# Kernel optimization log

Measured on AMD Instinct MI355X. Metric: run time of the kernel, lower is better.

The kernel has to match this reference:

```python
import jax, jax.numpy as jnp
import numpy as np

N_AGENT = 25
N_S = 32
N_A = 4
HID = 128
EHH_HID = HID * N_AGENT          # 3200
INTER = 150                      # INTERMEDIATE_NODES
BATCH = 2048
N_EDGE = 300


def _leaky(x):
    return jnp.where(x >= 0, x, 0.01 * x)


def setup_inputs() -> dict:
    key = jax.random.key(0)
    ks = jax.random.split(key, 12)
    states = jax.random.normal(ks[0], (N_AGENT, BATCH, N_S), dtype=jnp.float32)
    ehh_w = jax.random.normal(ks[1], (N_AGENT * N_S, EHH_HID), dtype=jnp.float32) * 0.05
    anova = jax.random.normal(ks[2], (EHH_HID + INTER, N_AGENT), dtype=jnp.float32)
    w1 = jax.random.normal(ks[3], (N_AGENT, EHH_HID, 12), dtype=jnp.float32) * 0.02
    b1 = jax.random.normal(ks[4], (N_AGENT, 12), dtype=jnp.float32) * 0.02
    w2 = jax.random.normal(ks[5], (N_AGENT, 12, 12), dtype=jnp.float32) * 0.3
    b2 = jax.random.normal(ks[6], (N_AGENT, 12), dtype=jnp.float32) * 0.02
    w3 = jax.random.normal(ks[7], (N_AGENT, 12, N_A), dtype=jnp.float32) * 0.3
    b3 = jax.random.normal(ks[8], (N_AGENT, N_A), dtype=jnp.float32) * 0.02
    actions = jax.random.randint(ks[9], (N_AGENT, BATCH), 0, N_A, dtype=jnp.int32)
    # adjacency rows: (bi_att_row, neighbor_row_a, unused, neighbor_row_b)
    c0 = jax.random.randint(ks[10], (N_EDGE, 1), 0, INTER, dtype=jnp.int32)
    c13 = jax.random.randint(ks[11], (N_EDGE, 2), 0, EHH_HID, dtype=jnp.int32)
    adj = jnp.concatenate([c0, c13[:, :1], jnp.zeros((N_EDGE, 1), jnp.int32), c13[:, 1:]], axis=1)
    return {"states": states, "ehh_w": ehh_w, "anova": anova,
            "w1": w1, "b1": b1, "w2": w2, "b2": b2, "w3": w3, "b3": b3,
            "actions": actions, "adj": adj}


def reference(states, ehh_w, anova, w1, b1, w2, b2, w3, b3, actions, adj):
    # states: (A, B, S) -> ehh_s: (B, A*S)   (torch.cat(states, dim=1))
    B = states.shape[1]
    ehh_s = jnp.transpose(states, (1, 0, 2)).reshape(B, -1)
    # EHH normalization (BatchNorm, affine=False, batch stats) + linear + LeakyReLU
    mu = jnp.mean(ehh_s, axis=0, keepdims=True)
    var = jnp.var(ehh_s, axis=0, keepdims=True)
    ehh_n = (ehh_s - mu) * jax.lax.rsqrt(var + 1e-5)
    ehh_embedding = _leaky(ehh_n @ ehh_w)                    # (B, EHH_HID)

    # ANOVA attention assembly via adjacency scatter
    self_att = anova[:EHH_HID, :]                            # (EHH_HID, A)
    bi_att = anova[EHH_HID:, :]                              # (INTER, A)
    vals = bi_att[adj[:, 0], :]                              # (E, A)
    neighbor_att = jnp.zeros((EHH_HID, N_AGENT), jnp.float32)
    neighbor_att = neighbor_att.at[adj[:, 1]].set(vals)
    neighbor_att = neighbor_att.at[adj[:, 3]].set(vals)
    all_att = (self_att + neighbor_att).T                    # (A, EHH_HID)

    # att_s repeat/permute/reshape == broadcast of embedding per agent
    att_out = ehh_embedding[:, None, :] * all_att[None, :, :]  # (B, A, EHH_HID)

    # per-agent critics (ehh_hidden -> 12 -> 12 -> n_a)
    h1 = _leaky(jnp.einsum('bah,ahk->bak', att_out, w1) + b1[None])
    h2 = _leaky(jnp.einsum('bak,akj->baj', h1, w2) + b2[None])
    all_q = jnp.einsum('baj,ajc->bac', h2, w3) + b3[None]     # (B, A, N_A)

    # q = all_q.gather(1, in_acs) per agent -> (A, B)
    q = jnp.take_along_axis(all_q, actions.T[:, :, None], axis=2)[..., 0].T
    return q
```

## Files before the change

kernel.cpp:

```cpp
#include <hip/hip_runtime.h>
#include <cstdint>

#define NAG 25
#define NS 32
#define EHH 3200
#define KDIM 800
#define BATCH 2048
#define NEDGE 300
#define NPAD 384
#define KSPLIT 5

typedef _Float16 half8 __attribute__((ext_vector_type(8)));
typedef float f32x4 __attribute__((ext_vector_type(4)));

__device__ __forceinline__ float leaky(float x) { return x >= 0.f ? x : 0.01f * x; }

__global__ void init_kernel(float* __restrict__ acc, int* __restrict__ winner) {
    int t = blockIdx.x * 256 + threadIdx.x;
    if (t < 1600) acc[t] = 0.f;
    if (t < EHH) winner[t] = -1;
}

__global__ void stats_part(const float* __restrict__ states, float* __restrict__ acc) {
    int a = blockIdx.x;
    int chunk = blockIdx.y;
    int s = threadIdx.x & 31, ty = threadIdx.x >> 5;
    const float* base = states + ((size_t)a * BATCH + chunk * 128) * NS + s;
    float sum = 0.f, sq = 0.f;
    for (int b = ty; b < 128; b += 8) {
        float v = base[(size_t)b * NS];
        sum += v; sq += v * v;
    }
    __shared__ float ls[8][32], lq[8][32];
    ls[ty][s] = sum; lq[ty][s] = sq;
    __syncthreads();
    if (ty == 0) {
#pragma unroll
        for (int i = 1; i < 8; ++i) { sum += ls[i][s]; sq += lq[i][s]; }
        atomicAdd(&acc[a * 32 + s], sum);
        atomicAdd(&acc[800 + a * 32 + s], sq);
    }
}

__global__ void prep_kernel(const float* __restrict__ states, const float* __restrict__ acc,
                            const float* __restrict__ ehh_w, const int* __restrict__ adj,
                            int* __restrict__ winner,
                            _Float16* __restrict__ A, _Float16* __restrict__ wt) {
    __shared__ float tile[32][33];
    int bi = blockIdx.x;
    if (bi < 6400) {
        int t = bi * 256 + threadIdx.x;
        int b = t / KDIM;
        int f = t - b * KDIM;
        int a = f >> 5, s = f & 31;
        float m = acc[f] * (1.f / BATCH);
        float var = acc[800 + f] * (1.f / BATCH) - m * m;
        float rs = rsqrtf(var + 1e-5f);
        float v = states[((size_t)a * BATCH + b) * NS + s];
        A[t] = (_Float16)((v - m) * rs);
    } else if (bi < 8900) {
        int bb = bi - 6400;
        int n0 = (bb % 100) * 32, k0 = (bb / 100) * 32;
        int x = threadIdx.x & 31, y = threadIdx.x >> 5;
        for (int i = y; i < 32; i += 8)
            tile[i][x] = ehh_w[(size_t)(k0 + i) * EHH + n0 + x];
        __syncthreads();
        for (int i = y; i < 32; i += 8)
            wt[(size_t)(n0 + i) * KDIM + k0 + x] = (_Float16)tile[x][i];
    } else {
        int e = (bi - 8900) * 256 + threadIdx.x;
        if (e < 2 * NEDGE) {
            int pass = e >= NEDGE;
            int ee = pass ? e - NEDGE : e;
            int dest = adj[ee * 4 + (pass ? 3 : 1)];
            atomicMax(&winner[dest], e);
        }
    }
}

__global__ void w2d_kernel(const float* __restrict__ anova, const int* __restrict__ adj,
                           const int* __restrict__ winner, const float* __restrict__ w1,
                           _Float16* __restrict__ w2dt) {
    if (blockIdx.x < 313) {
        int t = blockIdx.x * 256 + threadIdx.x;
        if (t < NAG * EHH) {
            int a = t / EHH;
            int h = t - a * EHH;
            float att = anova[(size_t)h * NAG + a];
            int w = winner[h];
            if (w >= 0) {
                int ee = w >= NEDGE ? w - NEDGE : w;
                att += anova[(size_t)(EHH + adj[ee * 4]) * NAG + a];
            }
            const float* wp = w1 + ((size_t)a * EHH + h) * 12;
#pragma unroll
            for (int kk = 0; kk < 12; ++kk)
                w2dt[(size_t)(a * 12 + kk) * EHH + h] = (_Float16)(att * wp[kk]);
        }
    } else {
        int p = (blockIdx.x - 313) * 256 + threadIdx.x;
        if (p < (NPAD - 300) * EHH / 8) {
            half8 z = {0, 0, 0, 0, 0, 0, 0, 0};
            ((half8*)(w2dt + (size_t)300 * EHH))[p] = z;
        }
    }
}

__device__ __forceinline__ void async16(const void* g, void* l) {
    __builtin_amdgcn_global_load_lds(
        (const __attribute__((address_space(1))) void*)(uintptr_t)g,
        (__attribute__((address_space(3))) void*)(unsigned)(uintptr_t)l, 16, 0, 0);
}

template <bool LEAKY_F16_OUT>
__global__ __launch_bounds__(256)
void gemm_bt(const _Float16* __restrict__ A, const _Float16* __restrict__ B,
             _Float16* __restrict__ Ch, float* __restrict__ Cf,
             int Ktot, int ldc, int kPerSplit, int slabStride) {
    __shared__ __attribute__((aligned(16))) _Float16 As[2][128 * 32];
    __shared__ __attribute__((aligned(16))) _Float16 Bs[2][128 * 32];
    const int tid = threadIdx.x;
    const int lane = tid & 63;
    const int wave = tid >> 6;
    const int wm = (wave >> 1) << 6;
    const int wn = (wave & 1) << 6;
    const int m0 = blockIdx.x << 7;
    const int n0 = blockIdx.y << 7;
    const int k0 = blockIdx.z * kPerSplit;
    const int nk = kPerSplit >> 5;

    const int srow = lane >> 2;
    const int scol = (lane & 3) << 3;
    const _Float16* gA0 = A + (size_t)(m0 + wave * 16 + srow) * Ktot + k0 + scol;
    const _Float16* gA1 = gA0 + (size_t)64 * Ktot;
    const _Float16* gB0 = B + (size_t)(n0 + wave * 16 + srow) * Ktot + k0 + scol;
    const _Float16* gB1 = gB0 + (size_t)64 * Ktot;
    const int lofs = wave * 512;

    f32x4 acc[4][4];
    const f32x4 zero = {0.f, 0.f, 0.f, 0.f};
#pragma unroll
    for (int i = 0; i < 4; ++i)
#pragma unroll
        for (int j = 0; j < 4; ++j) acc[i][j] = zero;

    const int fr = lane & 15;
    const int q8 = (lane >> 4) << 3;

    async16(gA0, As[0] + lofs);
    async16(gA1, As[0] + 2048 + lofs);
    async16(gB0, Bs[0] + lofs);
    async16(gB1, Bs[0] + 2048 + lofs);

    for (int kt = 0; kt < nk; ++kt) {
        const int cur = kt & 1;
        __syncthreads();
        if (kt + 1 < nk) {
            const int ko = (kt + 1) << 5;
            const int nxt = cur ^ 1;
            async16(gA0 + ko, As[nxt] + lofs);
            async16(gA1 + ko, As[nxt] + 2048 + lofs);
            async16(gB0 + ko, Bs[nxt] + lofs);
            async16(gB1 + ko, Bs[nxt] + 2048 + lofs);
        }
        half8 av[4], bv[4];
#pragma unroll
        for (int i = 0; i < 4; ++i)
            av[i] = *(const half8*)(As[cur] + (wm + i * 16 + fr) * 32 + q8);
#pragma unroll
        for (int j = 0; j < 4; ++j)
            bv[j] = *(const half8*)(Bs[cur] + (wn + j * 16 + fr) * 32 + q8);
#pragma unroll
        for (int i = 0; i < 4; ++i)
#pragma unroll
            for (int j = 0; j < 4; ++j)
                acc[i][j] = __builtin_amdgcn_mfma_f32_16x16x32_f16(av[i], bv[j], acc[i][j], 0, 0, 0);
    }

    const int r0 = (lane >> 4) << 2;
    if (LEAKY_F16_OUT) {
#pragma unroll
        for (int i = 0; i < 4; ++i)
#pragma unroll
            for (int j = 0; j < 4; ++j)
#pragma unroll
                for (int r = 0; r < 4; ++r) {
                    int row = m0 + wm + i * 16 + r0 + r;
                    int col = n0 + wn + j * 16 + fr;
                    Ch[(size_t)row * ldc + col] = (_Float16)leaky(acc[i][j][r]);
                }
    } else {
        float* C = Cf + (size_t)blockIdx.z * slabStride;
#pragma unroll
        for (int i = 0; i < 4; ++i)
#pragma unroll
            for (int j = 0; j < 4; ++j)
#pragma unroll
                for (int r = 0; r < 4; ++r) {
                    int row = m0 + wm + i * 16 + r0 + r;
                    int col = n0 + wn + j * 16 + fr;
                    C[(size_t)row * ldc + col] = acc[i][j][r];
                }
    }
}

__global__ void tail_kernel(const float* __restrict__ Hp, const float* __restrict__ b1,
                            const float* __restrict__ w2, const float* __restrict__ b2,
                            const float* __restrict__ w3, const float* __restrict__ b3,
                            const int* __restrict__ act, float* __restrict__ out) {
    int t = blockIdx.x * 256 + threadIdx.x;
    int b = t & (BATCH - 1);
    int a = t >> 11;
    const float* hp = Hp + (size_t)b * NPAD + a * 12;
    float h1[12];
#pragma unroll
    for (int k = 0; k < 12; ++k) {
        float s = b1[a * 12 + k];
#pragma unroll
        for (int ks = 0; ks < KSPLIT; ++ks) s += hp[(size_t)ks * BATCH * NPAD + k];
        h1[k] = leaky(s);
    }
    float h2[12];
#pragma unroll
    for (int j = 0; j < 12; ++j) {
        float s = b2[a * 12 + j];
#pragma unroll
        for (int k = 0; k < 12; ++k) s += h1[k] * w2[(a * 12 + k) * 12 + j];
        h2[j] = leaky(s);
    }
    int c = act[t];
    float q = b3[a * 4 + c];
#pragma unroll
    for (int j = 0; j < 12; ++j) q += h2[j] * w3[(a * 12 + j) * 4 + c];
    out[t] = q;
}

extern "C" void kernel_launch(void* const* d_in, const int* in_sizes, int n_in,
                              void* d_out, int out_size, void* d_ws, size_t ws_size,
                              hipStream_t stream) {
    (void)in_sizes; (void)n_in; (void)out_size; (void)ws_size;
    const float* states = (const float*)d_in[0];
    const float* ehh_w  = (const float*)d_in[1];
    const float* anova  = (const float*)d_in[2];
    const float* w1     = (const float*)d_in[3];
    const float* b1     = (const float*)d_in[4];
    const float* w2     = (const float*)d_in[5];
    const float* b2     = (const float*)d_in[6];
    const float* w3     = (const float*)d_in[7];
    const float* b3     = (const float*)d_in[8];
    const int* actions  = (const int*)d_in[9];
    const int* adj      = (const int*)d_in[10];
    float* out = (float*)d_out;

    char* ws = (char*)d_ws;
    float*     acc    = (float*)    (ws + 0);
    int*       winner = (int*)      (ws + 8192);
    _Float16*  Abf    = (_Float16*) (ws + 32768);
    _Float16*  WbT    = (_Float16*) (ws + 3311616);
    _Float16*  W2dT   = (_Float16*) (ws + 8433664);
    _Float16*  emb    = (_Float16*) (ws + 10893312);
    float*     Hp     = (float*)    (ws + 24002560);

    init_kernel<<<13, 256, 0, stream>>>(acc, winner);
    stats_part<<<dim3(25, 16), 256, 0, stream>>>(states, acc);
    prep_kernel<<<8903, 256, 0, stream>>>(states, acc, ehh_w, adj, winner, Abf, WbT);
    w2d_kernel<<<445, 256, 0, stream>>>(anova, adj, winner, w1, W2dT);
    gemm_bt<true><<<dim3(16, 25, 1), 256, 0, stream>>>(Abf, WbT, emb, nullptr, KDIM, EHH, KDIM, 0);
    gemm_bt<false><<<dim3(16, 3, KSPLIT), 256, 0, stream>>>(emb, W2dT, nullptr, Hp, EHH, NPAD,
                                                            EHH / KSPLIT, BATCH * NPAD);
    tail_kernel<<<(BATCH * NAG) / 256, 256, 0, stream>>>(Hp, b1, w2, b2, w3, b3, actions, out);
}
```

Measured before the change: 142.3 us.

## Merge preprocessing kernels and compute BN stats without atomics

Replaces four preprocessing launches (init, stats, prep, w2d) with two: one kernel computes per-agent batch mean and rstd in a single block each, transposes ehh_w to fp16, and builds the attention-scaled W1 with a per-block shared-memory winner table. A second kernel normalizes states with vectorized 8-wide loads and stores. This removes launch overhead, global atomics and the separate zero-init pass, at the cost of each w2d block recomputing the 600-edge winner scatter redundantly in LDS.

```diff
diff --git a/kernel.cpp b/kernel.cpp
--- a/kernel.cpp
+++ b/kernel.cpp
@@ -15,95 +15,110 @@
 
 __device__ __forceinline__ float leaky(float x) { return x >= 0.f ? x : 0.01f * x; }
 
-__global__ void init_kernel(float* __restrict__ acc, int* __restrict__ winner) {
-    int t = blockIdx.x * 256 + threadIdx.x;
-    if (t < 1600) acc[t] = 0.f;
-    if (t < EHH) winner[t] = -1;
-}
-
-__global__ void stats_part(const float* __restrict__ states, float* __restrict__ acc) {
-    int a = blockIdx.x;
-    int chunk = blockIdx.y;
-    int s = threadIdx.x & 31, ty = threadIdx.x >> 5;
-    const float* base = states + ((size_t)a * BATCH + chunk * 128) * NS + s;
-    float sum = 0.f, sq = 0.f;
-    for (int b = ty; b < 128; b += 8) {
-        float v = base[(size_t)b * NS];
-        sum += v; sq += v * v;
-    }
-    __shared__ float ls[8][32], lq[8][32];
-    ls[ty][s] = sum; lq[ty][s] = sq;
-    __syncthreads();
-    if (ty == 0) {
-#pragma unroll
-        for (int i = 1; i < 8; ++i) { sum += ls[i][s]; sq += lq[i][s]; }
-        atomicAdd(&acc[a * 32 + s], sum);
-        atomicAdd(&acc[800 + a * 32 + s], sq);
-    }
-}
-
-__global__ void prep_kernel(const float* __restrict__ states, const float* __restrict__ acc,
-                            const float* __restrict__ ehh_w, const int* __restrict__ adj,
-                            int* __restrict__ winner,
-                            _Float16* __restrict__ A, _Float16* __restrict__ wt) {
+__global__ __launch_bounds__(256)
+void prep1_kernel(const float* __restrict__ states, const float* __restrict__ ehh_w,
+                  const int* __restrict__ adj, const float* __restrict__ anova,
+                  const float* __restrict__ w1,
+                  float* __restrict__ mean, float* __restrict__ rstd,
+                  _Float16* __restrict__ wt, _Float16* __restrict__ w2dt) {
+    __shared__ float redS[32][32];
+    __shared__ float redQ[32][32];
     __shared__ float tile[32][33];
-    int bi = blockIdx.x;
-    if (bi < 6400) {
-        int t = bi * 256 + threadIdx.x;
-        int b = t / KDIM;
-        int f = t - b * KDIM;
-        int a = f >> 5, s = f & 31;
-        float m = acc[f] * (1.f / BATCH);
-        float var = acc[800 + f] * (1.f / BATCH) - m * m;
-        float rs = rsqrtf(var + 1e-5f);
-        float v = states[((size_t)a * BATCH + b) * NS + s];
-        A[t] = (_Float16)((v - m) * rs);
-    } else if (bi < 8900) {
-        int bb = bi - 6400;
-        int n0 = (bb % 100) * 32, k0 = (bb / 100) * 32;
-        int x = threadIdx.x & 31, y = threadIdx.x >> 5;
+    __shared__ int win[EHH];
+    const int bi = blockIdx.x;
+    const int tid = threadIdx.x;
+
+    if (bi < 25) {
+        const int a = bi;
+        const int s4 = (tid & 7) << 2;
+        const int r0 = tid >> 3;
+        const float* base = states + ((size_t)a * BATCH + r0) * NS + s4;
+        f32x4 sum = {0.f, 0.f, 0.f, 0.f};
+        f32x4 sq  = {0.f, 0.f, 0.f, 0.f};
+#pragma unroll 8
+        for (int it = 0; it < 64; ++it) {
+            f32x4 v = *(const f32x4*)(base + (size_t)it * 32 * NS);
+            sum += v;
+            sq  += v * v;
+        }
+        *(f32x4*)&redS[r0][s4] = sum;
+        *(f32x4*)&redQ[r0][s4] = sq;
+        __syncthreads();
+        if (tid < 32) {
+            float s = 0.f, q = 0.f;
+#pragma unroll
+            for (int r = 0; r < 32; ++r) { s += redS[r][tid]; q += redQ[r][tid]; }
+            float m = s * (1.f / BATCH);
+            float var = q * (1.f / BATCH) - m * m;
+            mean[a * 32 + tid] = m;
+            rstd[a * 32 + tid] = rsqrtf(var + 1e-5f);
+        }
+    } else if (bi < 2525) {
+        const int bb = bi - 25;
+        const int n0 = (bb % 100) * 32, k0 = (bb / 100) * 32;
+        const int x = tid & 31, y = tid >> 5;
         for (int i = y; i < 32; i += 8)
             tile[i][x] = ehh_w[(size_t)(k0 + i) * EHH + n0 + x];
         __syncthreads();
         for (int i = y; i < 32; i += 8)
             wt[(size_t)(n0 + i) * KDIM + k0 + x] = (_Float16)tile[x][i];
     } else {
-        int e = (bi - 8900) * 256 + threadIdx.x;
-        if (e < 2 * NEDGE) {
-            int pass = e >= NEDGE;
-            int ee = pass ? e - NEDGE : e;
-            int dest = adj[ee * 4 + (pass ? 3 : 1)];
-            atomicMax(&winner[dest], e);
-        }
-    }
-}
-
-__global__ void w2d_kernel(const float* __restrict__ anova, const int* __restrict__ adj,
-                           const int* __restrict__ winner, const float* __restrict__ w1,
-                           _Float16* __restrict__ w2dt) {
-    if (blockIdx.x < 313) {
-        int t = blockIdx.x * 256 + threadIdx.x;
-        if (t < NAG * EHH) {
-            int a = t / EHH;
-            int h = t - a * EHH;
-            float att = anova[(size_t)h * NAG + a];
-            int w = winner[h];
-            if (w >= 0) {
-                int ee = w >= NEDGE ? w - NEDGE : w;
-                att += anova[(size_t)(EHH + adj[ee * 4]) * NAG + a];
+        const int bb = bi - 2525;
+        if (bb < 313) {
+            for (int h = tid; h < EHH; h += 256) win[h] = -1;
+            __syncthreads();
+            for (int e = tid; e < 2 * NEDGE; e += 256) {
+                int pass = e >= NEDGE;
+                int ee = pass ? e - NEDGE : e;
+                int dest = adj[ee * 4 + (pass ? 3 : 1)];
+                atomicMax(&win[dest], e);
             }
-            const float* wp = w1 + ((size_t)a * EHH + h) * 12;
-#pragma unroll
-            for (int kk = 0; kk < 12; ++kk)
-                w2dt[(size_t)(a * 12 + kk) * EHH + h] = (_Float16)(att * wp[kk]);
-        }
-    } else {
-        int p = (blockIdx.x - 313) * 256 + threadIdx.x;
-        if (p < (NPAD - 300) * EHH / 8) {
-            half8 z = {0, 0, 0, 0, 0, 0, 0, 0};
-            ((half8*)(w2dt + (size_t)300 * EHH))[p] = z;
-        }
-    }
+            __syncthreads();
+            int t = bb * 256 + tid;
+            if (t < NAG * EHH) {
+                int a = t / EHH;
+                int h = t - a * EHH;
+                float att = anova[(size_t)h * NAG + a];
+                int w = win[h];
+                if (w >= 0) {
+                    int ee = w >= NEDGE ? w - NEDGE : w;
+                    att += anova[(size_t)(EHH + adj[ee * 4]) * NAG + a];
+                }
+                const float* wp = w1 + ((size_t)a * EHH + h) * 12;
+#pragma unroll
+                for (int kk = 0; kk < 12; ++kk)
+                    w2dt[(size_t)(a * 12 + kk) * EHH + h] = (_Float16)(att * wp[kk]);
+            }
+        } else {
+            int p = (bb - 313) * 256 + tid;
+            if (p < (NPAD - 300) * EHH / 8) {
+                half8 z = {0, 0, 0, 0, 0, 0, 0, 0};
+                ((half8*)(w2dt + (size_t)300 * EHH))[p] = z;
+            }
+        }
+    }
+}
+
+__global__ __launch_bounds__(256)
+void norm_kernel(const float* __restrict__ states, const float* __restrict__ mean,
+                 const float* __restrict__ rstd, _Float16* __restrict__ A) {
+    int u = blockIdx.x * 256 + threadIdx.x;
+    int b = u / 100;
+    int fo = (u - b * 100) * 8;
+    int a = fo >> 5, s = fo & 31;
+    const float* sp = states + ((size_t)a * BATCH + b) * NS + s;
+    f32x4 v0 = *(const f32x4*)sp;
+    f32x4 v1 = *(const f32x4*)(sp + 4);
+    f32x4 m0 = *(const f32x4*)(mean + fo);
+    f32x4 m1 = *(const f32x4*)(mean + fo + 4);
+    f32x4 r0 = *(const f32x4*)(rstd + fo);
+    f32x4 r1 = *(const f32x4*)(rstd + fo + 4);
+    half8 out;
+#pragma unroll
+    for (int i = 0; i < 4; ++i) out[i] = (_Float16)((v0[i] - m0[i]) * r0[i]);
+#pragma unroll
+    for (int i = 0; i < 4; ++i) out[4 + i] = (_Float16)((v1[i] - m1[i]) * r1[i]);
+    *(half8*)(A + (size_t)b * KDIM + fo) = out;
 }
 
 __device__ __forceinline__ void async16(const void* g, void* l) {
@@ -253,18 +268,17 @@
     float* out = (float*)d_out;
 
     char* ws = (char*)d_ws;
-    float*     acc    = (float*)    (ws + 0);
-    int*       winner = (int*)      (ws + 8192);
+    float*     mean   = (float*)    (ws + 0);
+    float*     rstd   = (float*)    (ws + 4096);
     _Float16*  Abf    = (_Float16*) (ws + 32768);
     _Float16*  WbT    = (_Float16*) (ws + 3311616);
     _Float16*  W2dT   = (_Float16*) (ws + 8433664);
     _Float16*  emb    = (_Float16*) (ws + 10893312);
     float*     Hp     = (float*)    (ws + 24002560);
 
-    init_kernel<<<13, 256, 0, stream>>>(acc, winner);
-    stats_part<<<dim3(25, 16), 256, 0, stream>>>(states, acc);
-    prep_kernel<<<8903, 256, 0, stream>>>(states, acc, ehh_w, adj, winner, Abf, WbT);
-    w2d_kernel<<<445, 256, 0, stream>>>(anova, adj, winner, w1, W2dT);
+    prep1_kernel<<<2970, 256, 0, stream>>>(states, ehh_w, adj, anova, w1,
+                                           mean, rstd, WbT, W2dT);
+    norm_kernel<<<800, 256, 0, stream>>>(states, mean, rstd, Abf);
     gemm_bt<true><<<dim3(16, 25, 1), 256, 0, stream>>>(Abf, WbT, emb, nullptr, KDIM, EHH, KDIM, 0);
     gemm_bt<false><<<dim3(16, 3, KSPLIT), 256, 0, stream>>>(emb, W2dT, nullptr, Hp, EHH, NPAD,
                                                             EHH / KSPLIT, BATCH * NPAD);
```

After: 133.4 us. 6.3% less time.
